# Kernel optimization log

Hardware: AMD Instinct MI355X
Metric: run time of the kernel (lower is better)

The kernel has to match this reference:

```python
import jax, jax.numpy as jnp
import numpy as np

B, N, D = 2, 256, 128
LN_EPS = 1e-5


def _linear_params(key, d, scale):
    kw, kb = jax.random.split(key)
    W = jax.random.normal(kw, (d, d), jnp.float32) * scale
    b = jax.random.normal(kb, (d,), jnp.float32) * 0.02
    return W, b


def setup_inputs() -> dict:
    key = jax.random.key(0)
    ks = jax.random.split(key, 8)
    hidden_states = jax.random.normal(ks[0], (B, N, D), jnp.float32)
    structure_matrix = jax.random.normal(ks[1], (B, N, N, D), jnp.float32)
    scale = 1.0 / np.sqrt(D).astype(np.float32)
    Wq, bq = _linear_params(ks[2], D, scale)
    Wk, bk = _linear_params(ks[3], D, scale)
    Wv, bv = _linear_params(ks[4], D, scale)
    Wo, bo = _linear_params(ks[5], D, scale)
    ln_g = jnp.ones((D,), jnp.float32)
    ln_b = jnp.zeros((D,), jnp.float32)
    return dict(hidden_states=hidden_states, structure_matrix=structure_matrix,
                Wq=Wq, bq=bq, Wk=Wk, bk=bk, Wv=Wv, bv=bv, Wo=Wo, bo=bo,
                ln_g=ln_g, ln_b=ln_b)


def reference(hidden_states, structure_matrix, Wq, bq, Wk, bk, Wv, bv, Wo, bo, ln_g, ln_b):
    # hidden_states is accepted by the original forward but never used.
    d = structure_matrix.shape[-1]
    q = structure_matrix @ Wq + bq  # [B,N,N,D]
    k = structure_matrix @ Wk + bk
    v = structure_matrix @ Wv + bv
    # scores[b,i,j,k] = <Q[b,i,k,:], K[b,i,j,:]> / sqrt(D)
    # (equivalent to the torch broadcast multiply+sum, expressed as batched GEMM)
    scores = jnp.einsum('bikd,bijd->bijk', q, k) / jnp.sqrt(jnp.asarray(d, scores_dtype := q.dtype))
    probs = jax.nn.relu(scores)  # dropout is identity in eval mode
    # context[b,i,j,d] = sum_k probs[b,i,j,k] * V[b,i,k,d]
    ctx = jnp.einsum('bijk,bikd->bijd', probs, v)
    out = ctx @ Wo + bo
    x = out + structure_matrix  # residual
    mu = jnp.mean(x, axis=-1, keepdims=True)
    var = jnp.var(x, axis=-1, keepdims=True)
    return (x - mu) * jax.lax.rsqrt(var + LN_EPS) * ln_g + ln_b
```

## Files before the change

### kernel.cpp

```cpp
#include <hip/hip_runtime.h>

#define DEV static __device__ __forceinline__

typedef __bf16 bf16x8 __attribute__((ext_vector_type(8)));
typedef float  f32x16 __attribute__((ext_vector_type(16)));

DEV int rowmap(int r, int hi) { return (r & 3) + 8 * (r >> 2) + 4 * hi; }

DEV int swzQ(int row, int col) {
  return row * 256 + (((((col >> 3) ^ (row & 15)) << 3) | (col & 7)) << 1);
}
DEV int swzV(int d, int k) {
  return d * 512 + (((((k >> 3) ^ (d & 31)) << 3) | (k & 7)) << 1);
}

DEV unsigned pack2(float lo, float hi) {
  union { __bf16 h[2]; unsigned u; } x;
  x.h[0] = (__bf16)lo; x.h[1] = (__bf16)hi;
  return x.u;
}

DEV bf16x8 mk_frag(float d0, float d1, float d2, float d3,
                   float d4, float d5, float d6, float d7, int lane) {
  unsigned a0 = pack2(d0, d1), a1 = pack2(d2, d3);
  unsigned b0 = pack2(d4, d5), b1 = pack2(d6, d7);
  unsigned a0s = __shfl_xor(a0, 32), a1s = __shfl_xor(a1, 32);
  unsigned b0s = __shfl_xor(b0, 32), b1s = __shfl_xor(b1, 32);
  bool lo = lane < 32;
  union { unsigned u[4]; bf16x8 v; } r;
  r.u[0] = lo ? a0  : b0s;
  r.u[1] = lo ? a1  : b1s;
  r.u[2] = lo ? a0s : b0;
  r.u[3] = lo ? a1s : b1;
  return r.v;
}

DEV f32x16 fzero() {
  f32x16 z;
  #pragma unroll
  for (int i = 0; i < 16; ++i) z[i] = 0.f;
  return z;
}

DEV void copy_lds(char* dst, const char* src, int bytes, int tid) {
  for (int off = tid * 16; off < bytes; off += 512 * 16)
    *reinterpret_cast<int4*>(dst + off) = *reinterpret_cast<const int4*>(src + off);
}

DEV void stage_w32(const float* __restrict__ W, char* dst, int tid) {
  #pragma unroll
  for (int it = 0; it < 32; ++it) {
    int idx = tid + it * 512;
    int e = idx >> 7, dp = idx & 127;
    *reinterpret_cast<__bf16*>(dst + swzQ(dp, e)) = (__bf16)W[idx];
  }
}

DEV void proj32(const bf16x8 sf[8], const char* Wt, int ml, int hi, f32x16 acc[4]) {
  #pragma unroll
  for (int t = 0; t < 4; ++t) acc[t] = fzero();
  #pragma unroll
  for (int kk = 0; kk < 8; ++kk) {
    #pragma unroll
    for (int t = 0; t < 4; ++t) {
      bf16x8 wf = *reinterpret_cast<const bf16x8*>(
          Wt + swzQ(32 * t + ml, 16 * kk + 8 * hi));
      acc[t] = __builtin_amdgcn_mfma_f32_32x32x16_bf16(sf[kk], wf, acc[t], 0, 0, 0);
    }
  }
}

__global__ void prep_wt(const float* __restrict__ Wk, const float* __restrict__ Wq,
                        const float* __restrict__ Wv, const float* __restrict__ Wo,
                        __bf16* __restrict__ wt) {
  int idx = blockIdx.x * 256 + threadIdx.x;
  const float* W[4] = {Wk, Wq, Wv, Wo};
  int m = idx >> 14, rem = idx & 16383;
  int e = rem >> 7, dp = rem & 127;
  wt[m * 16384 + (swzQ(dp, e) >> 1)] = (__bf16)W[m][rem];
}

template<bool WS>
__global__ __launch_bounds__(512, 2)
void sapd_fused(const float* __restrict__ S,
                const float* __restrict__ bq, const float* __restrict__ bk,
                const float* __restrict__ bv, const float* __restrict__ bo,
                const float* __restrict__ Wq, const float* __restrict__ Wk,
                const float* __restrict__ Wv, const float* __restrict__ Wo,
                const float* __restrict__ lg, const float* __restrict__ lb,
                const __bf16* __restrict__ wt,
                float* __restrict__ out)
{
  extern __shared__ char smem[];
  char* QL = smem;
  char* VT = smem + 65536;

  const int tid  = threadIdx.x;
  const int lane = tid & 63;
  const int w    = tid >> 6;
  const int ml   = lane & 31;
  const int hi   = lane >> 5;
  const size_t sbase = (size_t)blockIdx.x * (256 * 128);
  const char* wsc = (const char*)wt;

  bf16x8 sfrag[8];
  {
    const float* srow = S + sbase + (size_t)(32 * w + ml) * 128;
    #pragma unroll
    for (int kk = 0; kk < 8; ++kk) {
      float4 a = *reinterpret_cast<const float4*>(srow + 16 * kk + 8 * hi);
      float4 b = *reinterpret_cast<const float4*>(srow + 16 * kk + 8 * hi + 4);
      bf16x8 f;
      f[0] = (__bf16)a.x; f[1] = (__bf16)a.y; f[2] = (__bf16)a.z; f[3] = (__bf16)a.w;
      f[4] = (__bf16)b.x; f[5] = (__bf16)b.y; f[6] = (__bf16)b.z; f[7] = (__bf16)b.w;
      sfrag[kk] = f;
    }
  }

  if (WS) {
    copy_lds(VT, wsc, 65536, tid);
  } else {
    stage_w32(Wk, VT, tid);
    stage_w32(Wq, VT + 32768, tid);
  }
  __syncthreads();

  f32x16 acc[4];
  char* KS = QL + w * 8192;

  proj32(sfrag, VT, ml, hi, acc);
  #pragma unroll
  for (int t = 0; t < 4; ++t) {
    float bb = bk[32 * t + ml];
    #pragma unroll
    for (int r = 0; r < 16; ++r)
      *reinterpret_cast<__bf16*>(KS + swzQ(rowmap(r, hi), 32 * t + ml)) =
          (__bf16)(acc[t][r] + bb);
  }
  bf16x8 kfrag[8];
  #pragma unroll
  for (int kk = 0; kk < 8; ++kk)
    kfrag[kk] = *reinterpret_cast<const bf16x8*>(KS + swzQ(ml, 16 * kk + 8 * hi));

  proj32(sfrag, VT + 32768, ml, hi, acc);
  #pragma unroll
  for (int t = 0; t < 4; ++t) {
    float bb = bq[32 * t + ml];
    #pragma unroll
    for (int r = 0; r < 16; ++r)
      *reinterpret_cast<__bf16*>(KS + swzQ(rowmap(r, hi), 32 * t + ml)) =
          (__bf16)(acc[t][r] + bb);
  }
  __syncthreads();

  if (WS) copy_lds(VT, wsc + 65536, 32768, tid);
  else    stage_w32(Wv, VT, tid);
  __syncthreads();

  proj32(sfrag, VT, ml, hi, acc);
  __syncthreads();
  #pragma unroll
  for (int t = 0; t < 4; ++t) {
    float bb = bv[32 * t + ml];
    int d = 32 * t + ml;
    #pragma unroll
    for (int p = 0; p < 8; ++p) {
      int k = 32 * w + rowmap(2 * p, hi);
      *reinterpret_cast<unsigned*>(VT + swzV(d, k)) =
          pack2(acc[t][2 * p] + bb, acc[t][2 * p + 1] + bb);
    }
  }
  __syncthreads();

  f32x16 ctx[4];
  #pragma unroll
  for (int m = 0; m < 4; ++m) ctx[m] = fzero();
  const float SC = 0.088388347648318447f;

  #pragma unroll 2
  for (int kt = 0; kt < 8; ++kt) {
    f32x16 sa = fzero();
    #pragma unroll
    for (int kk = 0; kk < 8; ++kk) {
      bf16x8 qf = *reinterpret_cast<const bf16x8*>(
          QL + swzQ(32 * kt + ml, 16 * kk + 8 * hi));
      sa = __builtin_amdgcn_mfma_f32_32x32x16_bf16(qf, kfrag[kk], sa, 0, 0, 0);
    }
    float p[16];
    #pragma unroll
    for (int r = 0; r < 16; ++r) p[r] = fmaxf(sa[r] * SC, 0.f);
    bf16x8 pf0 = mk_frag(p[0], p[1], p[2], p[3], p[4], p[5], p[6], p[7], lane);
    bf16x8 pf1 = mk_frag(p[8], p[9], p[10], p[11], p[12], p[13], p[14], p[15], lane);
    #pragma unroll
    for (int m = 0; m < 4; ++m) {
      bf16x8 vf0 = *reinterpret_cast<const bf16x8*>(
          VT + swzV(32 * m + ml, 32 * kt + 8 * hi));
      ctx[m] = __builtin_amdgcn_mfma_f32_32x32x16_bf16(vf0, pf0, ctx[m], 0, 0, 0);
      bf16x8 vf1 = *reinterpret_cast<const bf16x8*>(
          VT + swzV(32 * m + ml, 32 * kt + 16 + 8 * hi));
      ctx[m] = __builtin_amdgcn_mfma_f32_32x32x16_bf16(vf1, pf1, ctx[m], 0, 0, 0);
    }
  }

  bf16x8 cf[8];
  #pragma unroll
  for (int m = 0; m < 4; ++m) {
    cf[2 * m]     = mk_frag(ctx[m][0], ctx[m][1], ctx[m][2], ctx[m][3],
                            ctx[m][4], ctx[m][5], ctx[m][6], ctx[m][7], lane);
    cf[2 * m + 1] = mk_frag(ctx[m][8], ctx[m][9], ctx[m][10], ctx[m][11],
                            ctx[m][12], ctx[m][13], ctx[m][14], ctx[m][15], lane);
  }
  __syncthreads();
  if (WS) copy_lds(QL, wsc + 98304, 32768, tid);
  else    stage_w32(Wo, QL, tid);
  __syncthreads();

  f32x16 oa[4];
  #pragma unroll
  for (int t = 0; t < 4; ++t) oa[t] = fzero();
  #pragma unroll
  for (int kk = 0; kk < 8; ++kk) {
    #pragma unroll
    for (int t = 0; t < 4; ++t) {
      bf16x8 wf = *reinterpret_cast<const bf16x8*>(
          QL + swzQ(32 * t + ml, 16 * kk + 8 * hi));
      oa[t] = __builtin_amdgcn_mfma_f32_32x32x16_bf16(cf[kk], wf, oa[t], 0, 0, 0);
    }
  }

  float gg[4], lbv[4], bov[4];
  #pragma unroll
  for (int t = 0; t < 4; ++t) {
    gg[t]  = lg[32 * t + ml];
    lbv[t] = lb[32 * t + ml];
    bov[t] = bo[32 * t + ml];
  }
  float sum[16], ssq[16];
  #pragma unroll
  for (int r = 0; r < 16; ++r) { sum[r] = 0.f; ssq[r] = 0.f; }
  #pragma unroll
  for (int t = 0; t < 4; ++t) {
    #pragma unroll
    for (int r = 0; r < 16; ++r) {
      size_t off = sbase + (size_t)(32 * w + rowmap(r, hi)) * 128 + 32 * t + ml;
      float x = oa[t][r] + bov[t] + S[off];
      oa[t][r] = x;
      sum[r] += x;
      ssq[r] += x * x;
    }
  }
  #pragma unroll
  for (int r = 0; r < 16; ++r) {
    float s_ = sum[r], q_ = ssq[r];
    #pragma unroll
    for (int m = 1; m <= 16; m <<= 1) {
      s_ += __shfl_xor(s_, m);
      q_ += __shfl_xor(q_, m);
    }
    float mu = s_ * (1.f / 128.f);
    float var = q_ * (1.f / 128.f) - mu * mu;
    float rs = rsqrtf(var + 1e-5f);
    float* orow = out + sbase + (size_t)(32 * w + rowmap(r, hi)) * 128;
    #pragma unroll
    for (int t = 0; t < 4; ++t)
      orow[32 * t + ml] = (oa[t][r] - mu) * rs * gg[t] + lbv[t];
  }
}

extern "C" void kernel_launch(void* const* d_in, const int* in_sizes, int n_in,
                              void* d_out, int out_size, void* d_ws, size_t ws_size,
                              hipStream_t stream) {
  (void)in_sizes; (void)n_in; (void)out_size;
  const float* S  = (const float*)d_in[1];
  const float* Wq = (const float*)d_in[2];
  const float* bq = (const float*)d_in[3];
  const float* Wk = (const float*)d_in[4];
  const float* bk = (const float*)d_in[5];
  const float* Wv = (const float*)d_in[6];
  const float* bv = (const float*)d_in[7];
  const float* Wo = (const float*)d_in[8];
  const float* bo = (const float*)d_in[9];
  const float* lg = (const float*)d_in[10];
  const float* lb = (const float*)d_in[11];
  float* out = (float*)d_out;

  constexpr int SMEM = 131072;
  bool use_ws = (d_ws != nullptr) && (ws_size >= 131072);
  if (use_ws) {
    prep_wt<<<dim3(256), dim3(256), 0, stream>>>(Wk, Wq, Wv, Wo, (__bf16*)d_ws);
    (void)hipFuncSetAttribute(reinterpret_cast<const void*>(&sapd_fused<true>),
                              hipFuncAttributeMaxDynamicSharedMemorySize, SMEM);
    sapd_fused<true><<<dim3(512), dim3(512), SMEM, stream>>>(
        S, bq, bk, bv, bo, Wq, Wk, Wv, Wo, lg, lb, (const __bf16*)d_ws, out);
  } else {
    (void)hipFuncSetAttribute(reinterpret_cast<const void*>(&sapd_fused<false>),
                              hipFuncAttributeMaxDynamicSharedMemorySize, SMEM);
    sapd_fused<false><<<dim3(512), dim3(512), SMEM, stream>>>(
        S, bq, bk, bv, bo, Wq, Wk, Wv, Wo, lg, lb, nullptr, out);
  }
}
```

Measured before the change: 69.34 us.

## Stage all QKV weights up front via direct global-to-LDS loads and register K

Stages the K, Q and V weights into LDS at kernel start with direct global-to-LDS loads, overlapping that with the S fragment loads. Computes K transposed so its fragments are built in registers rather than round-tripped through LDS. Q, K and V projections now run back to back, which removes two barriers and one staging phase. Also prefetches the residual S values while Wo loads and raises the score-loop unroll. The cost is higher register pressure from three live accumulator sets plus the residual buffer, which may spill or cut occupancy.

After: 73.76 us. +6.4%, slower.

```diff
diff --git a/kernel.cpp b/kernel.cpp
--- a/kernel.cpp
+++ b/kernel.cpp
@@ -42,9 +42,10 @@
   return z;
 }
 
-DEV void copy_lds(char* dst, const char* src, int bytes, int tid) {
-  for (int off = tid * 16; off < bytes; off += 512 * 16)
-    *reinterpret_cast<int4*>(dst + off) = *reinterpret_cast<const int4*>(src + off);
+DEV void gld16(const char* g, char* l) {
+  __builtin_amdgcn_global_load_lds(
+      (const __attribute__((address_space(1))) void*)g,
+      (__attribute__((address_space(3))) void*)l, 16, 0, 0);
 }
 
 DEV void stage_w32(const float* __restrict__ W, char* dst, int tid) {
@@ -53,20 +54,6 @@
     int idx = tid + it * 512;
     int e = idx >> 7, dp = idx & 127;
     *reinterpret_cast<__bf16*>(dst + swzQ(dp, e)) = (__bf16)W[idx];
-  }
-}
-
-DEV void proj32(const bf16x8 sf[8], const char* Wt, int ml, int hi, f32x16 acc[4]) {
-  #pragma unroll
-  for (int t = 0; t < 4; ++t) acc[t] = fzero();
-  #pragma unroll
-  for (int kk = 0; kk < 8; ++kk) {
-    #pragma unroll
-    for (int t = 0; t < 4; ++t) {
-      bf16x8 wf = *reinterpret_cast<const bf16x8*>(
-          Wt + swzQ(32 * t + ml, 16 * kk + 8 * hi));
-      acc[t] = __builtin_amdgcn_mfma_f32_32x32x16_bf16(sf[kk], wf, acc[t], 0, 0, 0);
-    }
   }
 }
 
@@ -103,6 +90,19 @@
   const size_t sbase = (size_t)blockIdx.x * (256 * 128);
   const char* wsc = (const char*)wt;
 
+  if (WS) {
+    #pragma unroll
+    for (int j = 0; j < 12; ++j) {
+      int c = w + 8 * j;
+      char* dst = (c < 64) ? (VT + c * 1024) : (QL + (c - 64) * 1024);
+      gld16(wsc + c * 1024 + lane * 16, dst);
+    }
+  } else {
+    stage_w32(Wk, VT, tid);
+    stage_w32(Wq, VT + 32768, tid);
+    stage_w32(Wv, QL, tid);
+  }
+
   bf16x8 sfrag[8];
   {
     const float* srow = S + sbase + (size_t)(32 * w + ml) * 128;
@@ -116,49 +116,67 @@
       sfrag[kk] = f;
     }
   }
-
-  if (WS) {
-    copy_lds(VT, wsc, 65536, tid);
-  } else {
-    stage_w32(Wk, VT, tid);
-    stage_w32(Wq, VT + 32768, tid);
-  }
-  __syncthreads();
-
-  f32x16 acc[4];
-  char* KS = QL + w * 8192;
-
-  proj32(sfrag, VT, ml, hi, acc);
-  #pragma unroll
-  for (int t = 0; t < 4; ++t) {
-    float bb = bk[32 * t + ml];
+  __syncthreads();
+
+  f32x16 accK[4];
+  #pragma unroll
+  for (int t = 0; t < 4; ++t) accK[t] = fzero();
+  #pragma unroll
+  for (int kk = 0; kk < 8; ++kk) {
+    #pragma unroll
+    for (int t = 0; t < 4; ++t) {
+      bf16x8 wf = *reinterpret_cast<const bf16x8*>(
+          VT + swzQ(32 * t + ml, 16 * kk + 8 * hi));
+      accK[t] = __builtin_amdgcn_mfma_f32_32x32x16_bf16(wf, sfrag[kk], accK[t], 0, 0, 0);
+    }
+  }
+  bf16x8 kfrag[8];
+  #pragma unroll
+  for (int t = 0; t < 4; ++t) {
+    #pragma unroll
+    for (int r = 0; r < 16; ++r) accK[t][r] += bk[32 * t + rowmap(r, hi)];
+    kfrag[2 * t]     = mk_frag(accK[t][0], accK[t][1], accK[t][2], accK[t][3],
+                               accK[t][4], accK[t][5], accK[t][6], accK[t][7], lane);
+    kfrag[2 * t + 1] = mk_frag(accK[t][8], accK[t][9], accK[t][10], accK[t][11],
+                               accK[t][12], accK[t][13], accK[t][14], accK[t][15], lane);
+  }
+
+  f32x16 accQ[4];
+  #pragma unroll
+  for (int t = 0; t < 4; ++t) accQ[t] = fzero();
+  #pragma unroll
+  for (int kk = 0; kk < 8; ++kk) {
+    #pragma unroll
+    for (int t = 0; t < 4; ++t) {
+      bf16x8 wf = *reinterpret_cast<const bf16x8*>(
+          VT + 32768 + swzQ(32 * t + ml, 16 * kk + 8 * hi));
+      accQ[t] = __builtin_amdgcn_mfma_f32_32x32x16_bf16(sfrag[kk], wf, accQ[t], 0, 0, 0);
+    }
+  }
+
+  f32x16 accV[4];
+  #pragma unroll
+  for (int t = 0; t < 4; ++t) accV[t] = fzero();
+  #pragma unroll
+  for (int kk = 0; kk < 8; ++kk) {
+    #pragma unroll
+    for (int t = 0; t < 4; ++t) {
+      bf16x8 wf = *reinterpret_cast<const bf16x8*>(
+          QL + swzQ(32 * t + ml, 16 * kk + 8 * hi));
+      accV[t] = __builtin_amdgcn_mfma_f32_32x32x16_bf16(sfrag[kk], wf, accV[t], 0, 0, 0);
+    }
+  }
+  __syncthreads();
+
+  #pragma unroll
+  for (int t = 0; t < 4; ++t) {
+    float bb = bq[32 * t + ml];
     #pragma unroll
     for (int r = 0; r < 16; ++r)
-      *reinterpret_cast<__bf16*>(KS + swzQ(rowmap(r, hi), 32 * t + ml)) =
-          (__bf16)(acc[t][r] + bb);
-  }
-  bf16x8 kfrag[8];
-  #pragma unroll
-  for (int kk = 0; kk < 8; ++kk)
-    kfrag[kk] = *reinterpret_cast<const bf16x8*>(KS + swzQ(ml, 16 * kk + 8 * hi));
-
-  proj32(sfrag, VT + 32768, ml, hi, acc);
-  #pragma unroll
-  for (int t = 0; t < 4; ++t) {
-    float bb = bq[32 * t + ml];
-    #pragma unroll
-    for (int r = 0; r < 16; ++r)
-      *reinterpret_cast<__bf16*>(KS + swzQ(rowmap(r, hi), 32 * t + ml)) =
-          (__bf16)(acc[t][r] + bb);
-  }
-  __syncthreads();
-
-  if (WS) copy_lds(VT, wsc + 65536, 32768, tid);
-  else    stage_w32(Wv, VT, tid);
-  __syncthreads();
-
-  proj32(sfrag, VT, ml, hi, acc);
-  __syncthreads();
+      *reinterpret_cast<__bf16*>(
+          QL + swzQ(32 * w + rowmap(r, hi), 32 * t + ml)) =
+          (__bf16)(accQ[t][r] + bb);
+  }
   #pragma unroll
   for (int t = 0; t < 4; ++t) {
     float bb = bv[32 * t + ml];
@@ -167,7 +185,7 @@
     for (int p = 0; p < 8; ++p) {
       int k = 32 * w + rowmap(2 * p, hi);
       *reinterpret_cast<unsigned*>(VT + swzV(d, k)) =
-          pack2(acc[t][2 * p] + bb, acc[t][2 * p + 1] + bb);
+          pack2(accV[t][2 * p] + bb, accV[t][2 * p + 1] + bb);
     }
   }
   __syncthreads();
@@ -177,7 +195,7 @@
   for (int m = 0; m < 4; ++m) ctx[m] = fzero();
   const float SC = 0.088388347648318447f;
 
-  #pragma unroll 2
+  #pragma unroll 4
   for (int kt = 0; kt < 8; ++kt) {
     f32x16 sa = fzero();
     #pragma unroll
@@ -211,8 +229,22 @@
                             ctx[m][12], ctx[m][13], ctx[m][14], ctx[m][15], lane);
   }
   __syncthreads();
-  if (WS) copy_lds(QL, wsc + 98304, 32768, tid);
-  else    stage_w32(Wo, QL, tid);
+  if (WS) {
+    #pragma unroll
+    for (int j = 0; j < 4; ++j) {
+      int c = w + 8 * j;
+      gld16(wsc + 98304 + c * 1024 + lane * 16, QL + c * 1024);
+    }
+  } else {
+    stage_w32(Wo, QL, tid);
+  }
+  float resv[4][16];
+  #pragma unroll
+  for (int t = 0; t < 4; ++t) {
+    #pragma unroll
+    for (int r = 0; r < 16; ++r)
+      resv[t][r] = S[sbase + (size_t)(32 * w + rowmap(r, hi)) * 128 + 32 * t + ml];
+  }
   __syncthreads();
 
   f32x16 oa[4];
@@ -242,8 +274,7 @@
   for (int t = 0; t < 4; ++t) {
     #pragma unroll
     for (int r = 0; r < 16; ++r) {
-      size_t off = sbase + (size_t)(32 * w + rowmap(r, hi)) * 128 + 32 * t + ml;
-      float x = oa[t][r] + bov[t] + S[off];
+      float x = oa[t][r] + bov[t] + resv[t][r];
       oa[t][r] = x;
       sum[r] += x;
       ssq[r] += x * x;
```
